# Performance work log

Measured on AMD Instinct MI355X. Metric: run time of the kernel, lower is better.

The kernel has to match this reference:

```python
import jax, jax.numpy as jnp
import numpy as np

B, N, H = 32, 100, 32
D = N * H
DEG = 3          # Chebyshev degree
GRID_SIZE, K = 5, 3  # B-spline grid size and order
WIN, STEP = 10, 2

def _laplacian(m):
    # calculate_laplacian_with_self_loop: D^-1/2 (A+I)^T D^-1/2
    m = m + jnp.eye(m.shape[0], dtype=m.dtype)
    d = jnp.power(m.sum(1), -0.5)
    d = jnp.where(jnp.isinf(d), 0.0, d)
    return (m * d[None, :]).T * d[None, :]

def setup_inputs() -> dict:
    key = jax.random.key(0)
    ks = jax.random.split(key, 12)
    adj = jax.random.uniform(ks[0], (N, N)); adj = (adj + adj.T) * 0.5
    cor = jax.random.uniform(ks[1], (N, N)); cor = (cor + cor.T) * 0.5
    lim = float(np.sqrt(6.0 / (H + 1 + H)))  # xavier_uniform for gc weights
    return {
        'inputs': jax.random.normal(ks[2], (B, N), jnp.float32),
        'hidden_state': jax.random.normal(ks[3], (B, N, H), jnp.float32),
        'laplacian': _laplacian(adj),
        'corr': _laplacian(cor),
        'gc_w': jax.random.uniform(ks[4], (H + 1, H), jnp.float32, -lim, lim),
        'gc_b': jnp.ones((H,), jnp.float32),  # bias init 1.0
        'ln_g': jnp.ones((H,), jnp.float32),
        'ln_b': jnp.zeros((H,), jnp.float32),
        'cheb_c': jax.random.normal(ks[5], (D, D, DEG + 1), jnp.float32) / np.sqrt(D * (DEG + 1)),
        'bkan_base_w': jax.random.normal(ks[6], (D, D), jnp.float32) / np.sqrt(D),
        'bkan_spline_w': jax.random.normal(ks[7], (D, D, GRID_SIZE + K), jnp.float32) / np.sqrt(D * (GRID_SIZE + K)),
        'taylor_c': jax.random.normal(ks[8], (D, D, 3), jnp.float32) / np.sqrt(D * 3),
        'min_p': jnp.float32(0.0), 'max_p': jnp.float32(1.0),
        'min_s': jnp.float32(0.0), 'max_s': jnp.float32(1.0),
        'min_n': jnp.float32(0.0), 'max_n': jnp.float32(1.0),
    }

def _unfold(x, size, step):
    nw = (x.shape[1] - size) // step + 1
    idx = jnp.arange(nw)[:, None] * step + jnp.arange(size)[None, :]
    return x[:, idx]  # [B, nw, size]

def _bspline_bases(x, grid, k):
    # Cox-de Boor recursion; x:[B,D], grid:[GRID_SIZE+2k+1]
    xg = x[..., None]
    b = ((xg >= grid[:-1]) & (xg < grid[1:])).astype(x.dtype)
    for d in range(1, k + 1):
        left = (xg - grid[:-(d + 1)]) / (grid[d:-1] - grid[:-(d + 1)]) * b[..., :-1]
        right = (grid[d + 1:] - xg) / (grid[d + 1:] - grid[1:-d]) * b[..., 1:]
        b = left + right
    return b  # [B, D, GRID_SIZE + k]

def _norm(s, lo, hi):
    return jnp.abs((s - lo) / (hi - lo + 1e-8))

def _forward(inputs, hidden_state, laplacian, corr, gc_w, gc_b, ln_g, ln_b,
             cheb_c, bkan_base_w, bkan_spline_w, taylor_c,
             min_p, max_p, min_s, max_s, min_n, max_n):
    # --- adaptive graph convolution ---
    alpha = jax.nn.sigmoid(inputs.mean(0))  # [N]
    A = alpha[None, :] * laplacian + (1.0 - alpha[None, :]) * corr  # broadcast over rows (torch semantics)
    concat = jnp.concatenate([inputs[..., None], hidden_state], axis=2)  # [B,N,H+1]
    ax = jnp.einsum('mn,bnf->bmf', A, concat)
    h = jnp.einsum('bnf,fo->bno', ax, gc_w) + gc_b  # [B,N,H]
    # --- layer norm over hidden dim ---
    mu = h.mean(-1, keepdims=True)
    var = ((h - mu) ** 2).mean(-1, keepdims=True)
    h = (h - mu) / jnp.sqrt(var + 1e-5) * ln_g + ln_b
    hs = h.reshape(B, D)
    # --- gating scores ---
    unf = _unfold(hs, WIN, STEP)
    p = _norm(jnp.abs(jnp.fft.fft(unf, axis=-1)).mean((-1, -2)), min_p, max_p)
    s = 1.0 - _norm(jnp.abs(jnp.diff(unf, axis=-1)).mean((-1, -2)), min_s, max_s)
    n = _norm(jnp.abs(jnp.diff(jnp.diff(hs, axis=1), axis=1)).mean(-1), min_n, max_n)
    gates = jax.nn.softmax(jnp.abs(jnp.stack([p, s, n], axis=1)), axis=1)  # [B,3]
    xc = gates[:, 0:1] * hs
    xb = gates[:, 1:2] * hs
    xt = gates[:, 2:3] * hs
    # --- Chebyshev KAN expert ---
    theta = jnp.arccos(jnp.tanh(xc))
    cb = jnp.cos(theta[..., None] * jnp.arange(DEG + 1, dtype=hs.dtype))  # [B,D,DEG+1]
    yc = jnp.einsum('bid,iod->bo', cb, cheb_c)
    # --- B-spline KAN expert ---
    grid = jnp.arange(-K, GRID_SIZE + K + 1, dtype=hs.dtype) * (2.0 / GRID_SIZE) - 1.0
    sb = _bspline_bases(xb, grid, K)  # [B,D,GRID_SIZE+K]
    yb = jax.nn.silu(xb) @ bkan_base_w.T + jnp.einsum('bik,oik->bo', sb, bkan_spline_w)
    # --- Taylor KAN expert (powers 1..3) ---
    pw = jnp.stack([xt, xt ** 2, xt ** 3], axis=-1)  # [B,D,3]
    yt = jnp.einsum('bip,iop->bo', pw, taylor_c)
    return (yc + yb + yt).reshape(B, N, H)

def reference(inputs, hidden_state, laplacian, corr, gc_w, gc_b, ln_g, ln_b,
              cheb_c, bkan_base_w, bkan_spline_w, taylor_c,
              min_p, max_p, min_s, max_s, min_n, max_n):
    return _forward(inputs, hidden_state, laplacian, corr, gc_w, gc_b, ln_g, ln_b,
                    cheb_c, bkan_base_w, bkan_spline_w, taylor_c,
                    min_p, max_p, min_s, max_s, min_n, max_n)
```

## Files before the change

kernel.cpp:

```cpp
#include <hip/hip_runtime.h>
#include <cmath>

#define DF 3200
#define NB 32
#define NN 100

#define OFF_ALPHA 0
#define OFF_GATES 128
#define OFF_HS    256
#define OFF_CB    (OFF_HS + NB*DF)
#define OFF_PW    (OFF_CB + NB*DF*4)
#define OFF_SILU  (OFF_PW + NB*DF*4)
#define OFF_SB    (OFF_SILU + NB*DF)

__global__ void k0_alpha(const float* __restrict__ inp, float* __restrict__ ws) {
    int n = threadIdx.x;
    if (n < NN) {
        float s = 0.f;
        for (int b = 0; b < NB; b++) s += inp[b * NN + n];
        s *= (1.0f / NB);
        ws[OFF_ALPHA + n] = 1.0f / (1.0f + expf(-s));
    }
}

__global__ void k1_gcln(const float* __restrict__ inp, const float* __restrict__ hid,
                        const float* __restrict__ lap, const float* __restrict__ corr,
                        const float* __restrict__ gcw, const float* __restrict__ gcb,
                        const float* __restrict__ lng, const float* __restrict__ lnb,
                        float* __restrict__ ws) {
    int bm = blockIdx.x;
    int b = bm / NN, m = bm % NN;
    __shared__ float axs[33];
    __shared__ float hsh[32];
    const float* alpha = ws + OFF_ALPHA;
    int f = threadIdx.x;
    if (f < 33) {
        float s = 0.f;
        for (int n = 0; n < NN; n++) {
            float a = alpha[n];
            float A = a * lap[m * NN + n] + (1.0f - a) * corr[m * NN + n];
            float c = (f == 0) ? inp[b * NN + n] : hid[(b * NN + n) * 32 + (f - 1)];
            s += A * c;
        }
        axs[f] = s;
    }
    __syncthreads();
    int o = threadIdx.x;
    if (o < 32) {
        float h = gcb[o];
        for (int ff = 0; ff < 33; ff++) h += axs[ff] * gcw[ff * 32 + o];
        hsh[o] = h;
    }
    __syncthreads();
    if (o < 32) {
        float mu = 0.f;
        for (int j = 0; j < 32; j++) mu += hsh[j];
        mu *= (1.f / 32.f);
        float var = 0.f;
        for (int j = 0; j < 32; j++) { float d = hsh[j] - mu; var += d * d; }
        var *= (1.f / 32.f);
        float v = (hsh[o] - mu) / sqrtf(var + 1e-5f) * lng[o] + lnb[o];
        ws[OFF_HS + b * DF + m * 32 + o] = v;
    }
}

__global__ void k2_gates(float* __restrict__ ws,
                         const float* __restrict__ minp, const float* __restrict__ maxp,
                         const float* __restrict__ mins, const float* __restrict__ maxs,
                         const float* __restrict__ minn, const float* __restrict__ maxn) {
    int b = blockIdx.x, t = threadIdx.x;
    const float* hs = ws + OFF_HS + (long)b * DF;
    __shared__ float c10[10], s10[10];
    __shared__ float red[12];
    if (t < 10) {
        float ang = 0.62831853071795864769f * (float)t;
        c10[t] = cosf(ang);
        s10[t] = sinf(ang);
    }
    __syncthreads();
    float psum = 0.f, ssum = 0.f, nsum = 0.f;
    const int NWIN = (DF - 10) / 2 + 1;
    for (int w = t; w < NWIN; w += 256) {
        float x[10];
#pragma unroll
        for (int j = 0; j < 10; j++) x[j] = hs[w * 2 + j];
#pragma unroll
        for (int k = 0; k < 10; k++) {
            float re = 0.f, im = 0.f;
#pragma unroll
            for (int j = 0; j < 10; j++) {
                int m = (j * k) % 10;
                re += x[j] * c10[m];
                im += x[j] * s10[m];
            }
            psum += sqrtf(re * re + im * im);
        }
#pragma unroll
        for (int j = 0; j < 9; j++) ssum += fabsf(x[j + 1] - x[j]);
    }
    for (int d = t; d < DF - 2; d += 256)
        nsum += fabsf(hs[d + 2] - 2.0f * hs[d + 1] + hs[d]);
    for (int off = 32; off > 0; off >>= 1) {
        psum += __shfl_down(psum, off, 64);
        ssum += __shfl_down(ssum, off, 64);
        nsum += __shfl_down(nsum, off, 64);
    }
    int lane = t & 63, wid = t >> 6;
    if (lane == 0) { red[wid] = psum; red[4 + wid] = ssum; red[8 + wid] = nsum; }
    __syncthreads();
    if (t == 0) {
        float pt = red[0] + red[1] + red[2] + red[3];
        float st = red[4] + red[5] + red[6] + red[7];
        float nt = red[8] + red[9] + red[10] + red[11];
        float pm = pt / (float)(NWIN * 10);
        float sm = st / (float)(NWIN * 9);
        float nm = nt / (float)(DF - 2);
        float p = fabsf((pm - *minp) / (*maxp - *minp + 1e-8f));
        float s = 1.0f - fabsf((sm - *mins) / (*maxs - *mins + 1e-8f));
        float n = fabsf((nm - *minn) / (*maxn - *minn + 1e-8f));
        float a0 = fabsf(p), a1 = fabsf(s), a2 = fabsf(n);
        float mx = fmaxf(a0, fmaxf(a1, a2));
        float e0 = expf(a0 - mx), e1 = expf(a1 - mx), e2 = expf(a2 - mx);
        float inv = 1.0f / (e0 + e1 + e2);
        ws[OFF_GATES + b * 4 + 0] = e0 * inv;
        ws[OFF_GATES + b * 4 + 1] = e1 * inv;
        ws[OFF_GATES + b * 4 + 2] = e2 * inv;
    }
}

__device__ __forceinline__ float gv(int j) { return 0.4f * (float)(j - 3) - 1.0f; }

__global__ void k3_feat(float* __restrict__ ws) {
    int q = blockIdx.x * 256 + threadIdx.x;
    int i = q >> 5, b = q & 31;
    float x = ws[OFF_HS + (long)b * DF + i];
    float g0 = ws[OFF_GATES + b * 4 + 0];
    float g1 = ws[OFF_GATES + b * 4 + 1];
    float g2 = ws[OFF_GATES + b * 4 + 2];
    float xc = g0 * x;
    float tt = tanhf(xc);
    float4 cb;
    cb.x = 1.0f;
    cb.y = tt;
    cb.z = 2.0f * tt * tt - 1.0f;
    cb.w = (4.0f * tt * tt - 3.0f) * tt;
    ((float4*)(ws + OFF_CB))[q] = cb;
    float xt = g2 * x;
    float4 pw;
    pw.x = xt; pw.y = xt * xt; pw.z = xt * xt * xt; pw.w = 0.f;
    ((float4*)(ws + OFF_PW))[q] = pw;
    float xb = g1 * x;
    ws[OFF_SILU + q] = xb / (1.0f + expf(-xb));
    float prev[11], cur[11];
#pragma unroll
    for (int j = 0; j < 11; j++)
        prev[j] = (xb >= gv(j) && xb < gv(j + 1)) ? 1.0f : 0.0f;
#pragma unroll
    for (int d = 1; d <= 3; d++) {
#pragma unroll
        for (int j = 0; j + d < 11; j++) {
            float l = (xb - gv(j)) / (gv(j + d) - gv(j)) * prev[j];
            float r = (gv(j + d + 1) - xb) / (gv(j + d + 1) - gv(j + 1)) * prev[j + 1];
            cur[j] = l + r;
        }
#pragma unroll
        for (int j = 0; j + d < 11; j++) prev[j] = cur[j];
    }
    float4 s0, s1;
    s0.x = prev[0]; s0.y = prev[1]; s0.z = prev[2]; s0.w = prev[3];
    s1.x = prev[4]; s1.y = prev[5]; s1.z = prev[6]; s1.w = prev[7];
    ((float4*)(ws + OFF_SB))[q * 2 + 0] = s0;
    ((float4*)(ws + OFF_SB))[q * 2 + 1] = s1;
}

__global__ __launch_bounds__(256) void e1_cheb_taylor(
        const float* __restrict__ cheb, const float* __restrict__ tay,
        const float* __restrict__ ws, float* __restrict__ out) {
    int o = blockIdx.x * 256 + threadIdx.x;
    bool valid = (o < DF);
    int i0 = blockIdx.y * 80;
    const float* cbf = ws + OFF_CB;
    const float* pwf = ws + OFF_PW;
    float acc[32];
#pragma unroll
    for (int b = 0; b < 32; b++) acc[b] = 0.f;
    for (int i = i0; i < i0 + 80; i++) {
        float4 w4 = {0.f, 0.f, 0.f, 0.f};
        float t0 = 0.f, t1 = 0.f, t2 = 0.f;
        if (valid) {
            w4 = *(const float4*)(cheb + ((long)i * DF + o) * 4);
            const float* tp = tay + ((long)i * DF + o) * 3;
            t0 = tp[0]; t1 = tp[1]; t2 = tp[2];
        }
        const float4* cp = (const float4*)cbf + (long)i * 32;
        const float4* pp = (const float4*)pwf + (long)i * 32;
#pragma unroll
        for (int b = 0; b < 32; b++) {
            float4 c = cp[b];
            float4 p = pp[b];
            acc[b] += w4.x * c.x + w4.y * c.y + w4.z * c.z + w4.w * c.w
                    + t0 * p.x + t1 * p.y + t2 * p.z;
        }
    }
    if (valid) {
#pragma unroll
        for (int b = 0; b < 32; b++) atomicAdd(out + (long)b * DF + o, acc[b]);
    }
}

__global__ __launch_bounds__(256) void e2_spline(
        const float* __restrict__ spw, const float* __restrict__ ws,
        float* __restrict__ out) {
    __shared__ float lds[256 * 36];
    int t = threadIdx.x;
    int o0 = blockIdx.x * 256;
    int o = o0 + t;
    bool valid = (o < DF);
    int ibase = blockIdx.y * 80;
    const float* sbf = ws + OFF_SB;
    float acc[32];
#pragma unroll
    for (int b = 0; b < 32; b++) acc[b] = 0.f;
    for (int ic = 0; ic < 80; ic += 4) {
        int i0 = ibase + ic;
        __syncthreads();
#pragma unroll
        for (int r = 0; r < 8; r++) {
            int q = r * 256 + t;
            int col = q >> 3, part = q & 7;
            int oc = o0 + col;
            float4 v = {0.f, 0.f, 0.f, 0.f};
            if (oc < DF) v = *(const float4*)(spw + ((long)oc * DF + i0) * 8 + part * 4);
            *(float4*)(lds + col * 36 + part * 4) = v;
        }
        __syncthreads();
#pragma unroll
        for (int ii = 0; ii < 4; ii++) {
            int i = i0 + ii;
            float4 wa = *(const float4*)(lds + t * 36 + ii * 8);
            float4 wb = *(const float4*)(lds + t * 36 + ii * 8 + 4);
            const float4* sp = (const float4*)(sbf + (long)i * 256);
#pragma unroll
            for (int b = 0; b < 32; b++) {
                float4 u0 = sp[2 * b];
                float4 u1 = sp[2 * b + 1];
                acc[b] += wa.x * u0.x + wa.y * u0.y + wa.z * u0.z + wa.w * u0.w
                        + wb.x * u1.x + wb.y * u1.y + wb.z * u1.z + wb.w * u1.w;
            }
        }
    }
    if (valid) {
#pragma unroll
        for (int b = 0; b < 32; b++) atomicAdd(out + (long)b * DF + o, acc[b]);
    }
}

__global__ __launch_bounds__(256) void e3_base(
        const float* __restrict__ bw, const float* __restrict__ ws,
        float* __restrict__ out) {
    __shared__ float lds[256 * 36];
    int t = threadIdx.x;
    int o0 = blockIdx.x * 256;
    int o = o0 + t;
    bool valid = (o < DF);
    int ibase = blockIdx.y * 128;
    const float* slf = ws + OFF_SILU;
    float acc[32];
#pragma unroll
    for (int b = 0; b < 32; b++) acc[b] = 0.f;
    for (int ic = 0; ic < 128; ic += 32) {
        int i0 = ibase + ic;
        __syncthreads();
#pragma unroll
        for (int r = 0; r < 8; r++) {
            int q = r * 256 + t;
            int col = q >> 3, part = q & 7;
            int oc = o0 + col;
            float4 v = {0.f, 0.f, 0.f, 0.f};
            if (oc < DF) v = *(const float4*)(bw + (long)oc * DF + i0 + part * 4);
            *(float4*)(lds + col * 36 + part * 4) = v;
        }
        __syncthreads();
        for (int ii = 0; ii < 32; ii++) {
            float w = lds[t * 36 + ii];
            const float* sl = slf + (long)(i0 + ii) * 32;
#pragma unroll
            for (int b = 0; b < 32; b++) acc[b] += w * sl[b];
        }
    }
    if (valid) {
#pragma unroll
        for (int b = 0; b < 32; b++) atomicAdd(out + (long)b * DF + o, acc[b]);
    }
}

extern "C" void kernel_launch(void* const* d_in, const int* in_sizes, int n_in,
                              void* d_out, int out_size, void* d_ws, size_t ws_size,
                              hipStream_t stream) {
    const float* inp  = (const float*)d_in[0];
    const float* hid  = (const float*)d_in[1];
    const float* lap  = (const float*)d_in[2];
    const float* corr = (const float*)d_in[3];
    const float* gcw  = (const float*)d_in[4];
    const float* gcb  = (const float*)d_in[5];
    const float* lng  = (const float*)d_in[6];
    const float* lnb  = (const float*)d_in[7];
    const float* cheb = (const float*)d_in[8];
    const float* bw   = (const float*)d_in[9];
    const float* spw  = (const float*)d_in[10];
    const float* tay  = (const float*)d_in[11];
    const float* minp = (const float*)d_in[12];
    const float* maxp = (const float*)d_in[13];
    const float* mins = (const float*)d_in[14];
    const float* maxs = (const float*)d_in[15];
    const float* minn = (const float*)d_in[16];
    const float* maxn = (const float*)d_in[17];
    float* out = (float*)d_out;
    float* ws  = (float*)d_ws;

    hipMemsetAsync(d_out, 0, (size_t)out_size * sizeof(float), stream);

    k0_alpha<<<1, 128, 0, stream>>>(inp, ws);
    k1_gcln<<<NB * NN, 64, 0, stream>>>(inp, hid, lap, corr, gcw, gcb, lng, lnb, ws);
    k2_gates<<<NB, 256, 0, stream>>>(ws, minp, maxp, mins, maxs, minn, maxn);
    k3_feat<<<(NB * DF) / 256, 256, 0, stream>>>(ws);

    e1_cheb_taylor<<<dim3(13, 40), 256, 0, stream>>>(cheb, tay, ws, out);
    e2_spline<<<dim3(13, 40), 256, 0, stream>>>(spw, ws, out);
    e3_base<<<dim3(13, 25), 256, 0, stream>>>(bw, ws, out);
}
```

Baseline: 1.238 ms.

## Stage feature tiles in LDS with register prefetch and double the i-split grid

The three expert GEMV-like kernels now stage the per-batch feature vectors in shared memory instead of reading them from global memory in the inner loop. Each chunk's weights and features are prefetched into registers while the current chunk is computed. The input dimension is split into twice as many blocks with occupancy hints of four blocks per CU, to raise parallelism and hide weight-streaming latency. The cost is more atomicAdd traffic to the output and extra register pressure from the prefetch buffers.

```diff
diff --git a/kernel.cpp b/kernel.cpp
--- a/kernel.cpp
+++ b/kernel.cpp
@@ -173,33 +173,66 @@
     ((float4*)(ws + OFF_SB))[q * 2 + 1] = s1;
 }
 
-__global__ __launch_bounds__(256) void e1_cheb_taylor(
+__global__ __launch_bounds__(256, 4) void e1_cheb_taylor(
         const float* __restrict__ cheb, const float* __restrict__ tay,
         const float* __restrict__ ws, float* __restrict__ out) {
-    int o = blockIdx.x * 256 + threadIdx.x;
+    __shared__ float lcb[4 * 32 * 4];
+    __shared__ float lpw[4 * 32 * 4];
+    int t = threadIdx.x;
+    int o = blockIdx.x * 256 + t;
     bool valid = (o < DF);
-    int i0 = blockIdx.y * 80;
-    const float* cbf = ws + OFF_CB;
-    const float* pwf = ws + OFF_PW;
+    int oo = valid ? o : DF - 1;
+    int ibase = blockIdx.y * 40;
+    const int NCH = 10;
+    const float4* cbsrc = (const float4*)(ws + OFF_CB);
+    const float4* pwsrc = (const float4*)(ws + OFF_PW);
+
     float acc[32];
 #pragma unroll
     for (int b = 0; b < 32; b++) acc[b] = 0.f;
-    for (int i = i0; i < i0 + 80; i++) {
-        float4 w4 = {0.f, 0.f, 0.f, 0.f};
-        float t0 = 0.f, t1 = 0.f, t2 = 0.f;
-        if (valid) {
-            w4 = *(const float4*)(cheb + ((long)i * DF + o) * 4);
-            const float* tp = tay + ((long)i * DF + o) * 3;
-            t0 = tp[0]; t1 = tp[1]; t2 = tp[2];
-        }
-        const float4* cp = (const float4*)cbf + (long)i * 32;
-        const float4* pp = (const float4*)pwf + (long)i * 32;
-#pragma unroll
-        for (int b = 0; b < 32; b++) {
-            float4 c = cp[b];
-            float4 p = pp[b];
-            acc[b] += w4.x * c.x + w4.y * c.y + w4.z * c.z + w4.w * c.w
-                    + t0 * p.x + t1 * p.y + t2 * p.z;
+
+    float4 wc[4]; float ty0[4], ty1[4], ty2[4]; float4 fpre;
+    {
+        int i0 = ibase;
+#pragma unroll
+        for (int ii = 0; ii < 4; ii++) {
+            wc[ii] = *(const float4*)(cheb + ((long)(i0 + ii) * DF + oo) * 4);
+            const float* tp = tay + ((long)(i0 + ii) * DF + oo) * 3;
+            ty0[ii] = tp[0]; ty1[ii] = tp[1]; ty2[ii] = tp[2];
+        }
+        fpre = (t < 128) ? cbsrc[(long)i0 * 32 + t] : pwsrc[(long)i0 * 32 + (t - 128)];
+    }
+
+    for (int c = 0; c < NCH; c++) {
+        __syncthreads();
+        if (t < 128) ((float4*)lcb)[t] = fpre;
+        else         ((float4*)lpw)[t - 128] = fpre;
+        float4 wcc[4]; float s0[4], s1[4], s2[4];
+#pragma unroll
+        for (int ii = 0; ii < 4; ii++) {
+            wcc[ii] = wc[ii]; s0[ii] = ty0[ii]; s1[ii] = ty1[ii]; s2[ii] = ty2[ii];
+        }
+        if (c + 1 < NCH) {
+            int i0 = ibase + (c + 1) * 4;
+#pragma unroll
+            for (int ii = 0; ii < 4; ii++) {
+                wc[ii] = *(const float4*)(cheb + ((long)(i0 + ii) * DF + oo) * 4);
+                const float* tp = tay + ((long)(i0 + ii) * DF + oo) * 3;
+                ty0[ii] = tp[0]; ty1[ii] = tp[1]; ty2[ii] = tp[2];
+            }
+            fpre = (t < 128) ? cbsrc[(long)i0 * 32 + t] : pwsrc[(long)i0 * 32 + (t - 128)];
+        }
+        __syncthreads();
+#pragma unroll
+        for (int ii = 0; ii < 4; ii++) {
+#pragma unroll
+            for (int b = 0; b < 32; b++) {
+                float4 cv = ((const float4*)lcb)[ii * 32 + b];
+                float4 pv = ((const float4*)lpw)[ii * 32 + b];
+                acc[b] += wcc[ii].x * cv.x + wcc[ii].y * cv.y
+                        + wcc[ii].z * cv.z + wcc[ii].w * cv.w
+                        + s0[ii] * pv.x + s1[ii] * pv.y + s2[ii] * pv.z;
+            }
         }
     }
     if (valid) {
@@ -208,42 +241,65 @@
     }
 }
 
-__global__ __launch_bounds__(256) void e2_spline(
+__global__ __launch_bounds__(256, 4) void e2_spline(
         const float* __restrict__ spw, const float* __restrict__ ws,
         float* __restrict__ out) {
-    __shared__ float lds[256 * 36];
+    __shared__ float lw[256 * 36];
+    __shared__ float lf[4 * 32 * 8];
     int t = threadIdx.x;
     int o0 = blockIdx.x * 256;
     int o = o0 + t;
     bool valid = (o < DF);
-    int ibase = blockIdx.y * 80;
+    int ibase = blockIdx.y * 40;
+    const int NCH = 10;
     const float* sbf = ws + OFF_SB;
+
     float acc[32];
 #pragma unroll
     for (int b = 0; b < 32; b++) acc[b] = 0.f;
-    for (int ic = 0; ic < 80; ic += 4) {
-        int i0 = ibase + ic;
-        __syncthreads();
+
+    float4 wpre[8]; float4 fpre;
+    {
+        int i0 = ibase;
 #pragma unroll
         for (int r = 0; r < 8; r++) {
             int q = r * 256 + t;
             int col = q >> 3, part = q & 7;
-            int oc = o0 + col;
-            float4 v = {0.f, 0.f, 0.f, 0.f};
-            if (oc < DF) v = *(const float4*)(spw + ((long)oc * DF + i0) * 8 + part * 4);
-            *(float4*)(lds + col * 36 + part * 4) = v;
+            int oc = o0 + col; if (oc >= DF) oc = DF - 1;
+            wpre[r] = *(const float4*)(spw + ((long)oc * DF + i0) * 8 + part * 4);
+        }
+        fpre = ((const float4*)(sbf + (long)i0 * 256))[t];
+    }
+
+    for (int c = 0; c < NCH; c++) {
+        __syncthreads();
+#pragma unroll
+        for (int r = 0; r < 8; r++) {
+            int q = r * 256 + t;
+            int col = q >> 3, part = q & 7;
+            *(float4*)(lw + col * 36 + part * 4) = wpre[r];
+        }
+        ((float4*)lf)[t] = fpre;
+        if (c + 1 < NCH) {
+            int i0 = ibase + (c + 1) * 4;
+#pragma unroll
+            for (int r = 0; r < 8; r++) {
+                int q = r * 256 + t;
+                int col = q >> 3, part = q & 7;
+                int oc = o0 + col; if (oc >= DF) oc = DF - 1;
+                wpre[r] = *(const float4*)(spw + ((long)oc * DF + i0) * 8 + part * 4);
+            }
+            fpre = ((const float4*)(sbf + (long)i0 * 256))[t];
         }
         __syncthreads();
 #pragma unroll
         for (int ii = 0; ii < 4; ii++) {
-            int i = i0 + ii;
-            float4 wa = *(const float4*)(lds + t * 36 + ii * 8);
-            float4 wb = *(const float4*)(lds + t * 36 + ii * 8 + 4);
-            const float4* sp = (const float4*)(sbf + (long)i * 256);
+            float4 wa = *(const float4*)(lw + t * 36 + ii * 8);
+            float4 wb = *(const float4*)(lw + t * 36 + ii * 8 + 4);
 #pragma unroll
             for (int b = 0; b < 32; b++) {
-                float4 u0 = sp[2 * b];
-                float4 u1 = sp[2 * b + 1];
+                float4 u0 = ((const float4*)lf)[(ii * 32 + b) * 2];
+                float4 u1 = ((const float4*)lf)[(ii * 32 + b) * 2 + 1];
                 acc[b] += wa.x * u0.x + wa.y * u0.y + wa.z * u0.z + wa.w * u0.w
                         + wb.x * u1.x + wb.y * u1.y + wb.z * u1.z + wb.w * u1.w;
             }
@@ -255,37 +311,71 @@
     }
 }
 
-__global__ __launch_bounds__(256) void e3_base(
+__global__ __launch_bounds__(256, 4) void e3_base(
         const float* __restrict__ bw, const float* __restrict__ ws,
         float* __restrict__ out) {
-    __shared__ float lds[256 * 36];
+    __shared__ float lw[256 * 20];
+    __shared__ float lft[32 * 16];
     int t = threadIdx.x;
     int o0 = blockIdx.x * 256;
     int o = o0 + t;
     bool valid = (o < DF);
-    int ibase = blockIdx.y * 128;
+    int ibase = blockIdx.y * 64;
+    const int NCH = 4;
     const float* slf = ws + OFF_SILU;
+
     float acc[32];
 #pragma unroll
     for (int b = 0; b < 32; b++) acc[b] = 0.f;
-    for (int ic = 0; ic < 128; ic += 32) {
-        int i0 = ibase + ic;
-        __syncthreads();
-#pragma unroll
-        for (int r = 0; r < 8; r++) {
+
+    float4 wpre[4]; float4 fpre = {0.f, 0.f, 0.f, 0.f};
+    {
+        int i0 = ibase;
+#pragma unroll
+        for (int r = 0; r < 4; r++) {
             int q = r * 256 + t;
-            int col = q >> 3, part = q & 7;
-            int oc = o0 + col;
-            float4 v = {0.f, 0.f, 0.f, 0.f};
-            if (oc < DF) v = *(const float4*)(bw + (long)oc * DF + i0 + part * 4);
-            *(float4*)(lds + col * 36 + part * 4) = v;
-        }
-        __syncthreads();
-        for (int ii = 0; ii < 32; ii++) {
-            float w = lds[t * 36 + ii];
-            const float* sl = slf + (long)(i0 + ii) * 32;
-#pragma unroll
-            for (int b = 0; b < 32; b++) acc[b] += w * sl[b];
+            int col = q >> 2, part = q & 3;
+            int oc = o0 + col; if (oc >= DF) oc = DF - 1;
+            wpre[r] = *(const float4*)(bw + (long)oc * DF + i0 + part * 4);
+        }
+        if (t < 128) fpre = ((const float4*)(slf + (long)i0 * 32))[t];
+    }
+
+    for (int c = 0; c < NCH; c++) {
+        __syncthreads();
+#pragma unroll
+        for (int r = 0; r < 4; r++) {
+            int q = r * 256 + t;
+            int col = q >> 2, part = q & 3;
+            *(float4*)(lw + col * 20 + part * 4) = wpre[r];
+        }
+        if (t < 128) {
+            int idx = t * 4;
+            lft[((idx) & 31) * 16 + ((idx) >> 5)]         = fpre.x;
+            lft[((idx + 1) & 31) * 16 + ((idx + 1) >> 5)] = fpre.y;
+            lft[((idx + 2) & 31) * 16 + ((idx + 2) >> 5)] = fpre.z;
+            lft[((idx + 3) & 31) * 16 + ((idx + 3) >> 5)] = fpre.w;
+        }
+        if (c + 1 < NCH) {
+            int i0 = ibase + (c + 1) * 16;
+#pragma unroll
+            for (int r = 0; r < 4; r++) {
+                int q = r * 256 + t;
+                int col = q >> 2, part = q & 3;
+                int oc = o0 + col; if (oc >= DF) oc = DF - 1;
+                wpre[r] = *(const float4*)(bw + (long)oc * DF + i0 + part * 4);
+            }
+            if (t < 128) fpre = ((const float4*)(slf + (long)i0 * 32))[t];
+        }
+        __syncthreads();
+#pragma unroll
+        for (int g = 0; g < 4; g++) {
+            float4 w = *(const float4*)(lw + t * 20 + g * 4);
+#pragma unroll
+            for (int b = 0; b < 32; b++) {
+                float4 fv = ((const float4*)lft)[b * 4 + g];
+                acc[b] += w.x * fv.x + w.y * fv.y + w.z * fv.z + w.w * fv.w;
+            }
         }
     }
     if (valid) {
@@ -325,7 +415,7 @@
     k2_gates<<<NB, 256, 0, stream>>>(ws, minp, maxp, mins, maxs, minn, maxn);
     k3_feat<<<(NB * DF) / 256, 256, 0, stream>>>(ws);
 
-    e1_cheb_taylor<<<dim3(13, 40), 256, 0, stream>>>(cheb, tay, ws, out);
-    e2_spline<<<dim3(13, 40), 256, 0, stream>>>(spw, ws, out);
-    e3_base<<<dim3(13, 25), 256, 0, stream>>>(bw, ws, out);
-}
+    e1_cheb_taylor<<<dim3(13, 80), 256, 0, stream>>>(cheb, tay, ws, out);
+    e2_spline<<<dim3(13, 80), 256, 0, stream>>>(spw, ws, out);
+    e3_base<<<dim3(13, 50), 256, 0, stream>>>(bw, ws, out);
+}
```

After: 1.517 ms. 1.23x slower.
